# Kernel tuning notes

Hardware: AMD Instinct MI355X
Metric: run time of the kernel (lower is better)

Reference implementation:

```python
import jax, jax.numpy as jnp
import numpy as np

B, S, N = 8, 512, 2048   # batch, seq_len (=input_dim=output_dim), num_features (graph nodes)
HID = 512
K = 8                    # k_neighbors


def _construct_adj(x, k):
    """Faithful port of construct_graph: note the original normalizes the
    (1, N) mean-feature vector along dim=1 (whole-vector L2 norm), so the
    'similarity matrix' is actually the outer product v v^T / ||v||^2."""
    Bn, Sn, Nn = x.shape
    fv = x.mean(axis=1)                                  # (B, N)
    nf = fv / jnp.linalg.norm(fv, axis=1, keepdims=True)  # whole-row L2 normalize
    sim = nf[:, :, None] * nf[:, None, :]                # (B, N, N) outer product
    kk = min(k, Nn - 1)
    _, idx = jax.lax.top_k(sim, kk + 1)                  # (B, N, kk+1)
    idx = idx[..., 1:]                                   # drop the single largest (B, N, kk)
    b_ix = jnp.arange(Bn)[:, None, None]
    r_ix = jnp.arange(Nn)[None, :, None]
    adj = jnp.zeros((Bn, Nn, Nn), x.dtype).at[b_ix, r_ix, idx].set(1.0)
    adj = jnp.maximum(adj, jnp.swapaxes(adj, 1, 2))      # symmetrize (adj[idx, i] = 1)
    d = jnp.arange(Nn)
    adj = adj.at[:, d, d].set(1.0)                       # fill_diagonal_(1)
    return adj


def _gc(x, adj, W, b):
    """GraphConvLayer: degree-normalized adjacency bmm after linear."""
    deg = adj.sum(axis=2, keepdims=True)                 # (B, N, 1)
    deg = jnp.where(deg == 0, jnp.ones_like(deg), deg)
    h = x @ W.T + b                                      # (B, N, out)
    return jnp.einsum('bij,bjh->bih', adj / deg, h)


def setup_inputs() -> dict:
    key = jax.random.key(0)
    k0, k1, k2 = jax.random.split(key, 3)
    x = jax.random.normal(k0, (B, S, N), jnp.float32)
    W1 = jax.random.normal(k1, (HID, S), jnp.float32) * 0.02
    b1 = jnp.zeros((HID,), jnp.float32)
    W2 = jax.random.normal(k2, (S, HID), jnp.float32) * 0.02
    b2 = jnp.zeros((S,), jnp.float32)
    return {"x": x, "W1": W1, "b1": b1, "W2": W2, "b2": b2}


def reference(x, W1, b1, W2, b2):
    adj = _construct_adj(x, K)                           # (B, N, N)
    xr = jnp.swapaxes(x, 1, 2)                           # (B, N, S)
    h = jax.nn.relu(_gc(xr, adj, W1, b1))                # (B, N, HID); dropout is eval no-op
    h = _gc(h, adj, W2, b2)                              # (B, N, S)
    return jnp.swapaxes(h, 1, 2)                         # (B, S, N)
```

## Files before the change

kernel.cpp:

```cpp
#include <hip/hip_runtime.h>
#include <hip/hip_bf16.h>
#include <cstdint>

typedef unsigned short u16;
typedef __bf16 bf16x8 __attribute__((ext_vector_type(8)));
typedef float f32x4 __attribute__((ext_vector_type(4)));
typedef float f32x8 __attribute__((ext_vector_type(8)));
typedef unsigned short u16x4 __attribute__((ext_vector_type(4)));
typedef unsigned short u16x8 __attribute__((ext_vector_type(8)));

#define BB 8
#define SS 512
#define NN 2048
#define HH 512
#define MM (BB*NN)

__device__ inline u16 f2b(float f) {
  __hip_bfloat16 h = __float2bfloat16(f);
  return *reinterpret_cast<u16*>(&h);
}
__device__ inline float b2f(u16 u) {
  unsigned x = ((unsigned)u) << 16;
  return __uint_as_float(x);
}
__device__ inline f32x8 b2f8(u16x8 v) {
  f32x8 r;
  #pragma unroll
  for (int k = 0; k < 8; ++k) r[k] = b2f(v[k]);
  return r;
}

#define GLOAD16(g, l) __builtin_amdgcn_global_load_lds( \
    (const __attribute__((address_space(1))) void*)(g), \
    (__attribute__((address_space(3))) void*)(l), 16, 0, 0)

__device__ inline void remap_mn(int bid, int& m0, int& n0) {
  const int xcd = bid & 7, k = bid >> 3;
  m0 = (xcd * 16 + (k >> 2)) * 128;
  n0 = (k & 3) * 128;
}

__global__ __launch_bounds__(256) void k_prep(const float* __restrict__ x, u16* __restrict__ xr,
                       float* __restrict__ fvp,
                       const float* __restrict__ W1, const float* __restrict__ W2,
                       u16* __restrict__ w1b, u16* __restrict__ w2b,
                       float* __restrict__ xs ) {
  const int u = blockIdx.x;
  const int tid = threadIdx.x;
  if (u < 4096) {
    __shared__ float t[64][33];
    __shared__ float ps[8][32];
    const int tx = tid & 31, ty = tid >> 5;
    const int n0 = (u & 63) * 32, st = (u >> 6) & 7, b = u >> 9;
    const int s0 = st * 64;
    float acc = 0.f;
    #pragma unroll
    for (int i = ty; i < 64; i += 8) {
      float w = x[(size_t)b*SS*NN + (size_t)(s0+i)*NN + n0 + tx];
      t[i][tx] = w; acc += w;
    }
    ps[ty][tx] = acc;
    __syncthreads();
    if (ty == 0) {
      float s = 0.f;
      #pragma unroll
      for (int j = 0; j < 8; ++j) s += ps[j][tx];
      fvp[((size_t)(b*8 + st))*NN + n0 + tx] = s;
    }
    const int wtx = tid & 15, wty = tid >> 4;
    #pragma unroll
    for (int j = wty; j < 32; j += 16) {
      ushort4 o;
      o.x = f2b(t[wtx*4+0][j]); o.y = f2b(t[wtx*4+1][j]);
      o.z = f2b(t[wtx*4+2][j]); o.w = f2b(t[wtx*4+3][j]);
      *(ushort4*)(xr + ((size_t)b*NN + n0 + j)*SS + s0 + wtx*4) = o;
    }
    if (u < 96) {
      ((float4*)xs)[u*256 + tid] = make_float4(0.f, 0.f, 0.f, 0.f);
    }
  } else {
    const int b2v = u - 4096;
    const float* Wsrc = (b2v >= 256) ? W2 : W1;
    u16* wb = (b2v >= 256) ? w2b : w1b;
    const int off = (b2v & 255) * 1024;
    float4 v = ((const float4*)(Wsrc + off))[tid];
    ushort4 o; o.x = f2b(v.x); o.y = f2b(v.y); o.z = f2b(v.z); o.w = f2b(v.w);
    *(ushort4*)(wb + off + tid*4) = o;
  }
}

__global__ __launch_bounds__(256) void k_tops(const float* __restrict__ fvp, const u16* __restrict__ xr,
                       int* __restrict__ meta, int* __restrict__ rowfl, float* __restrict__ xs) {
  const int tid = threadIdx.x;
  if (blockIdx.x < BB) {
    const int b = blockIdx.x;
    __shared__ float v[NN];
    __shared__ unsigned long long wk[8];
    __shared__ unsigned long long winner[2];
    __shared__ int sel[18];
    __shared__ int scnt[12];
    __shared__ int ccnt[12];
    const int wv = tid >> 6, ln = tid & 63;

    float lv[8];
    {
      f32x4 a0 = {0,0,0,0}, a1 = {0,0,0,0};
      for (int sb_ = 0; sb_ < 8; ++sb_) {
        const f32x4* p = (const f32x4*)(fvp + ((size_t)(b*8 + sb_))*NN + tid*8);
        a0 += p[0]; a1 += p[1];
      }
      lv[0]=a0[0]; lv[1]=a0[1]; lv[2]=a0[2]; lv[3]=a0[3];
      lv[4]=a1[0]; lv[5]=a1[1]; lv[6]=a1[2]; lv[7]=a1[3];
    }
    #pragma unroll
    for (int j = 0; j < 8; ++j) v[tid*8+j] = lv[j];

    unsigned long long kD[8], kA[8];
    #pragma unroll
    for (int j = 0; j < 8; ++j) {
      unsigned u = __float_as_uint(lv[j]);
      u = (u & 0x80000000u) ? ~u : (u | 0x80000000u);
      unsigned idx = (unsigned)(tid*8 + j);
      kD[j] = ((unsigned long long)u << 32) | (0xFFFFFFFFu - idx);
      kA[j] = ((unsigned long long)(~u) << 32) | (0xFFFFFFFFu - idx);
    }
    unsigned mskD = 0, mskA = 0;
    for (int r = 0; r < 9; ++r) {
      unsigned long long bD = 0ull, bA = 0ull;
      #pragma unroll
      for (int j = 0; j < 8; ++j) {
        if (!((mskD >> j) & 1) && kD[j] > bD) bD = kD[j];
        if (!((mskA >> j) & 1) && kA[j] > bA) bA = kA[j];
      }
      #pragma unroll
      for (int o = 32; o > 0; o >>= 1) {
        unsigned long long oD = __shfl_xor(bD, o, 64);
        unsigned long long oA = __shfl_xor(bA, o, 64);
        if (oD > bD) bD = oD;
        if (oA > bA) bA = oA;
      }
      if (ln == 0) { wk[wv] = bD; wk[4+wv] = bA; }
      __syncthreads();
      if (tid == 0) {
        unsigned long long mD = wk[0], mA = wk[4];
        #pragma unroll
        for (int q = 1; q < 4; ++q) {
          if (wk[q] > mD) mD = wk[q];
          if (wk[4+q] > mA) mA = wk[4+q];
        }
        winner[0] = mD; winner[1] = mA;
        sel[r]   = (int)(0xFFFFFFFFu - (unsigned)mD);
        sel[9+r] = (int)(0xFFFFFFFFu - (unsigned)mA);
      }
      __syncthreads();
      unsigned iD = 0xFFFFFFFFu - (unsigned)winner[0];
      unsigned iA = 0xFFFFFFFFu - (unsigned)winner[1];
      if ((int)(iD >> 3) == tid) mskD |= 1u << (iD & 7);
      if ((int)(iA >> 3) == tid) mskA |= 1u << (iA & 7);
    }

    int cp = 0, cn = 0, cz = 0;
    #pragma unroll
    for (int j = 0; j < 8; ++j) { cp += (lv[j] > 0.f); cn += (lv[j] < 0.f); cz += (lv[j] == 0.f); }
    #pragma unroll
    for (int o = 32; o > 0; o >>= 1) { cp += __shfl_xor(cp, o, 64); cn += __shfl_xor(cn, o, 64); cz += __shfl_xor(cz, o, 64); }
    if (ln == 0) { ccnt[wv] = cp; ccnt[4+wv] = cn; ccnt[8+wv] = cz; }
    __syncthreads();
    if (tid == 0) {
      int CP = 0, CN = 0, CZ = 0;
      #pragma unroll
      for (int q = 0; q < 4; ++q) { CP += ccnt[q]; CN += ccnt[4+q]; CZ += ccnt[8+q]; }
      scnt[0] = CP; scnt[1] = CN; scnt[2] = CZ;
      for (int t2 = 3; t2 < 12; ++t2) scnt[t2] = 0;
      for (int r = 1; r < 9; ++r) {
        float wD = v[sel[r]];   scnt[3] += (wD > 0.f); scnt[4] += (wD < 0.f); scnt[5] += (wD == 0.f);
        float wA = v[sel[9+r]]; scnt[6] += (wA > 0.f); scnt[7] += (wA < 0.f); scnt[8] += (wA == 0.f);
        float wZ = v[r];        scnt[9] += (wZ > 0.f); scnt[10] += (wZ < 0.f); scnt[11] += (wZ == 0.f);
      }
    }
    __syncthreads();
    #pragma unroll
    for (int j = 0; j < 8; ++j) {
      const int i = tid*8 + j;
      float w = lv[j];
      int cls = (w > 0.f) ? 0 : ((w < 0.f) ? 1 : 2);
      int mD = 0, mA = 0;
      #pragma unroll
      for (int r = 1; r < 9; ++r) { mD |= (sel[r] == i); mA |= (sel[9+r] == i); }
      int mZ8 = (i >= 1 && i <= 8);
      rowfl[b*NN + i] = cls | (mD << 2) | (mA << 3) | (mZ8 << 4);
    }
    if (tid < 18) meta[b*32 + tid] = sel[tid];
    if (tid >= 18 && tid < 30) meta[b*32 + tid] = scnt[tid - 18];
    __syncthreads();
    #pragma unroll
    for (int half = 0; half < 2; ++half) {
      const int d = tid + half*256;
      float a[9];
      #pragma unroll
      for (int q = 0; q < 9; ++q) a[q] = 0.f;
      for (int r = 1; r < 9; ++r) {
        int iD = sel[r];   float wD = v[iD]; int cD = (wD>0.f)?0:((wD<0.f)?1:2);
        float vD = b2f(xr[((size_t)b*NN + iD)*512 + d]);
        int iA = sel[9+r]; float wA = v[iA]; int cA = (wA>0.f)?0:((wA<0.f)?1:2);
        float vA = b2f(xr[((size_t)b*NN + iA)*512 + d]);
        float wZ = v[r];   int cZ = (wZ>0.f)?0:((wZ<0.f)?1:2);
        float vZ = b2f(xr[((size_t)b*NN + r)*512 + d]);
        #pragma unroll
        for (int q = 0; q < 3; ++q) {
          a[q]   += (cD == q) ? vD : 0.f;
          a[3+q] += (cA == q) ? vA : 0.f;
          a[6+q] += (cZ == q) ? vZ : 0.f;
        }
      }
      #pragma unroll
      for (int q = 0; q < 9; ++q) xs[((size_t)b*12 + 3 + q)*512 + d] = a[q];
    }
  } else {
    const int u = blockIdx.x - 8, b = u >> 5, c = u & 31, n0 = c*64;
    __shared__ f32x8 red[12][64];
    __shared__ int scls[64];
    if (tid < 64) {
      float s = 0.f;
      for (int sb_ = 0; sb_ < 8; ++sb_) s += fvp[((size_t)(b*8 + sb_))*NN + n0 + tid];
      scls[tid] = (s > 0.f) ? 0 : ((s < 0.f) ? 1 : 2);
    }
    __syncthreads();
    const int fc = tid & 63, rg = tid >> 6;
    f32x8 sp = {0,0,0,0,0,0,0,0}, sn = sp, sz = sp;
    for (int it = 0; it < 16; ++it) {
      const int nr = rg + it*4;
      const int cls = scls[nr];
      f32x8 hf = b2f8(*(const u16x8*)(xr + ((size_t)b*NN + n0 + nr)*512 + fc*8));
      if (cls == 0) sp += hf; else if (cls == 1) sn += hf; else sz += hf;
    }
    red[0*4+rg][fc] = sp; red[1*4+rg][fc] = sn; red[2*4+rg][fc] = sz;
    __syncthreads();
    if (rg == 0) {
      sp = red[0][fc] + red[1][fc] + red[2][fc] + red[3][fc];
      sn = red[4][fc] + red[5][fc] + red[6][fc] + red[7][fc];
      sz = red[8][fc] + red[9][fc] + red[10][fc] + red[11][fc];
      #pragma unroll
      for (int j = 0; j < 8; ++j) {
        atomicAdd(&xs[((size_t)b*12 + 0)*512 + fc*8 + j], sp[j]);
        atomicAdd(&xs[((size_t)b*12 + 1)*512 + fc*8 + j], sn[j]);
        atomicAdd(&xs[((size_t)b*12 + 2)*512 + fc*8 + j], sz[j]);
      }
    }
  }
}

__global__ __launch_bounds__(256) void k_sums(const u16* __restrict__ g1, const int* __restrict__ meta,
                      const int* __restrict__ rowfl, float* __restrict__ g1s) {
  const int tid = threadIdx.x;
  if (blockIdx.x < BB) {
    const int b = blockIdx.x;
    const int* mb = meta + b*32;
    #pragma unroll
    for (int half = 0; half < 2; ++half) {
      const int d = tid + half*256;
      float a[9];
      #pragma unroll
      for (int q = 0; q < 9; ++q) a[q] = 0.f;
      for (int r = 1; r < 9; ++r) {
        int iD = mb[r];   int cD = rowfl[b*NN + iD] & 3;
        float vD = b2f(g1[((size_t)b*NN + iD)*512 + d]);
        int iA = mb[9+r]; int cA = rowfl[b*NN + iA] & 3;
        float vA = b2f(g1[((size_t)b*NN + iA)*512 + d]);
        int cZ = rowfl[b*NN + r] & 3;
        float vZ = b2f(g1[((size_t)b*NN + r)*512 + d]);
        #pragma unroll
        for (int q = 0; q < 3; ++q) {
          a[q]   += (cD == q) ? vD : 0.f;
          a[3+q] += (cA == q) ? vA : 0.f;
          a[6+q] += (cZ == q) ? vZ : 0.f;
        }
      }
      #pragma unroll
      for (int q = 0; q < 9; ++q) g1s[((size_t)b*12 + 3 + q)*512 + d] = a[q];
    }
  } else {
    const int u = blockIdx.x - 8, b = u >> 5, c = u & 31, n0 = c*64;
    __shared__ f32x8 red[12][64];
    __shared__ int scls[64];
    if (tid < 64) scls[tid] = rowfl[b*NN + n0 + tid] & 3;
    __syncthreads();
    const int fc = tid & 63, rg = tid >> 6;
    f32x8 sp = {0,0,0,0,0,0,0,0}, sn = sp, sz = sp;
    for (int it = 0; it < 16; ++it) {
      const int nr = rg + it*4;
      const int cls = scls[nr];
      f32x8 hf = b2f8(*(const u16x8*)(g1 + ((size_t)b*NN + n0 + nr)*512 + fc*8));
      if (cls == 0) sp += hf; else if (cls == 1) sn += hf; else sz += hf;
    }
    red[0*4+rg][fc] = sp; red[1*4+rg][fc] = sn; red[2*4+rg][fc] = sz;
    __syncthreads();
    if (rg == 0) {
      sp = red[0][fc] + red[1][fc] + red[2][fc] + red[3][fc];
      sn = red[4][fc] + red[5][fc] + red[6][fc] + red[7][fc];
      sz = red[8][fc] + red[9][fc] + red[10][fc] + red[11][fc];
      #pragma unroll
      for (int j = 0; j < 8; ++j) {
        atomicAdd(&g1s[((size_t)b*12 + 0)*512 + fc*8 + j], sp[j]);
        atomicAdd(&g1s[((size_t)b*12 + 1)*512 + fc*8 + j], sn[j]);
        atomicAdd(&g1s[((size_t)b*12 + 2)*512 + fc*8 + j], sz[j]);
      }
    }
  }
}

template<int MODE>
__global__ __launch_bounds__(256, 2) void k_gemmf(const u16* __restrict__ A, const u16* __restrict__ Bw,
                       const float* __restrict__ bias, const float* __restrict__ sums,
                       const int* __restrict__ meta, const int* __restrict__ rowfl,
                       void* __restrict__ outp) {
  __shared__ __align__(16) char SM[33152];
  u16* As  = (u16*)SM;
  u16* Bs  = (u16*)(SM + 8192);
  u16* xsb = (u16*)(SM + 16384);
  int* cnt = (int*)(SM + 33088);
  const int tid = threadIdx.x;
  const int w = tid >> 6, l = tid & 63;
  const int wm = w >> 1, wn = w & 1;
  int m0, n0; remap_mn(blockIdx.x, m0, n0);
  const int b = m0 >> 11;

  for (int i = tid; i < 12*512; i += 256) {
    const int s = i >> 9, k = i & 511;
    xsb[s*520 + k] = f2b(sums[(size_t)b*12*512 + i]);
  }
  for (int i = tid; i < 4*520; i += 256) xsb[12*520 + i] = 0;
  if (tid < 12) cnt[tid] = meta[b*32 + 18 + tid];

  f32x4 acc[4][4]; f32x4 accV[4];
  #pragma unroll
  for (int i = 0; i < 4; ++i) {
    accV[i] = (f32x4){0.f, 0.f, 0.f, 0.f};
    #pragma unroll
    for (int j = 0; j < 4; ++j) acc[i][j] = (f32x4){0.f, 0.f, 0.f, 0.f};
  }
  const int srow = l >> 2;
  const int sslot = (l & 3) ^ ((l >> 3) & 3);
  const int skk = sslot * 8;
  const int lr = l & 15;
  const int g = l >> 4;
  const int lkA = ((g ^ ((lr >> 1) & 3)) * 8);
  const int lk = g * 8;
  for (int kt = 0; kt < 512; kt += 32) {
    #pragma unroll
    for (int p = 0; p < 2; ++p) {
      const int q = w*2 + p;
      GLOAD16(A  + (size_t)(m0 + q*16 + srow)*512 + kt + skk, As + q*512);
      GLOAD16(Bw + (size_t)(n0 + q*16 + srow)*512 + kt + skk, Bs + q*512);
    }
    __syncthreads();
    bf16x8 af[4], bfr[4];
    #pragma unroll
    for (int i = 0; i < 4; ++i) af[i] = *(const bf16x8*)(As + (wm*64 + i*16 + lr)*32 + lkA);
    #pragma unroll
    for (int j = 0; j < 4; ++j) bfr[j] = *(const bf16x8*)(Bs + (wn*64 + j*16 + lr)*32 + lkA);
    #pragma unroll
    for (int i = 0; i < 4; ++i)
      #pragma unroll
      for (int j = 0; j < 4; ++j)
        acc[i][j] = __builtin_amdgcn_mfma_f32_16x16x32_bf16(bfr[j], af[i], acc[i][j], 0, 0, 0);
    if (wm == 0) {
      bf16x8 afx = *(const bf16x8*)(xsb + lr*520 + kt + lk);
      #pragma unroll
      for (int j = 0; j < 4; ++j)
        accV[j] = __builtin_amdgcn_mfma_f32_16x16x32_bf16(afx, bfr[j], accV[j], 0, 0, 0);
    }
    __syncthreads();
  }

  float* Vl = (float*)SM;
  if (wm == 0) {
    #pragma unroll
    for (int j = 0; j < 4; ++j) {
      const int c = wn*64 + j*16 + lr;
      const float bv = bias[n0 + c];
      #pragma unroll
      for (int r = 0; r < 4; ++r) {
        const int s = (l >> 4)*4 + r;
        if (s < 12) Vl[s*128 + c] = accV[j][r] + (float)cnt[s] * bv;
      }
    }
  }
  __syncthreads();

  int fl[4]; float rdg[4]; bool cs[4];
  const float* Vb[4];
  #pragma unroll
  for (int i = 0; i < 4; ++i) {
    const int m = m0 + wm*64 + i*16 + lr;
    const int f = rowfl[m];
    fl[i] = f;
    const int cls = f & 3;
    const int bD = (f >> 2) & 1, bA = (f >> 3) & 1, bZ = (f >> 4) & 1;
    const int rb = 3 + cls*3;
    const int c3c = bD*cnt[0] + bA*cnt[1] + bZ*cnt[2];
    const int c2c = cnt[rb] + cnt[rb+1] + cnt[rb+2] - bD*cnt[rb] - bA*cnt[rb+1] - bZ*cnt[rb+2];
    cs[i] = (cls == 0 && bD) || (cls == 1 && bA) || (cls == 2 && bZ);
    float deg = (float)(c3c + c2c) + (cs[i] ? 0.f : 1.f);
    if (deg < 1.f) deg = 1.f;
    rdg[i] = 1.f / deg;
    Vb[i] = Vl + rb*128;
  }

  if (MODE == 0) {
    u16* G = (u16*)outp;
    #pragma unroll
    for (int j = 0; j < 4; ++j) {
      const int dgb = n0 + wn*64 + j*16 + (l >> 4)*4;
      u16x4 o[4];
      #pragma unroll
      for (int r = 0; r < 4; ++r) {
        const int c = wn*64 + j*16 + (l >> 4)*4 + r;
        const float bv = bias[dgb + r];
        const float v0 = Vl[c], v1 = Vl[128 + c], v2 = Vl[256 + c];
        #pragma unroll
        for (int i = 0; i < 4; ++i) {
          const int f = fl[i];
          const float t0 = Vb[i][c], t1 = Vb[i][128 + c], t2 = Vb[i][256 + c];
          float c3 = ((f&4)?v0:0.f) + ((f&8)?v1:0.f) + ((f&16)?v2:0.f);
          float c2 = t0 + t1 + t2
                   - ((f&4)?t0:0.f) - ((f&8)?t1:0.f) - ((f&16)?t2:0.f);
          float val = (c3 + c2) * rdg[i];
          if (!cs[i]) val += (acc[i][j][r] + bv) * rdg[i];
          o[i][r] = f2b(fmaxf(val, 0.f));
        }
      }
      #pragma unroll
      for (int i = 0; i < 4; ++i)
        *(u16x4*)(G + (size_t)(m0 + wm*64 + i*16 + lr)*512 + dgb) = o[i];
    }
  } else {
    float* out = (float*)outp;
    float (*ep)[130] = (float(*)[130])(SM + 8192);
    const int nloc = m0 & 2047;
    for (int j = 0; j < 4; ++j) {
      #pragma unroll
      for (int r = 0; r < 4; ++r) {
        const int c = wn*64 + j*16 + (l >> 4)*4 + r;
        const float bv = bias[n0 + c];
        const float v0 = Vl[c], v1 = Vl[128 + c], v2 = Vl[256 + c];
        #pragma unroll
        for (int i = 0; i < 4; ++i) {
          const int f = fl[i];
          const float t0 = Vb[i][c], t1 = Vb[i][128 + c], t2 = Vb[i][256 + c];
          float c3 = ((f&4)?v0:0.f) + ((f&8)?v1:0.f) + ((f&16)?v2:0.f);
          float c2 = t0 + t1 + t2
                   - ((f&4)?t0:0.f) - ((f&8)?t1:0.f) - ((f&16)?t2:0.f);
          float val = (c3 + c2) * rdg[i];
          if (!cs[i]) val += (acc[i][j][r] + bv) * rdg[i];
          ep[wn*16 + (l >> 4)*4 + r][wm*64 + i*16 + lr] = val;
        }
      }
      __syncthreads();
      #pragma unroll
      for (int rr = 0; rr < 8; ++rr) {
        const int q = w*8 + rr;
        const int s = n0 + (q >> 4)*64 + j*16 + (q & 15);
        float2 v2 = *(const float2*)&ep[q][2*l];
        *(float2*)(out + ((size_t)b*SS + s)*NN + nloc + 2*l) = v2;
      }
      __syncthreads();
    }
  }
}

extern "C" void kernel_launch(void* const* d_in, const int* in_sizes, int n_in,
                              void* d_out, int out_size, void* d_ws, size_t ws_size,
                              hipStream_t stream) {
  const float* x  = (const float*)d_in[0];
  const float* W1 = (const float*)d_in[1];
  const float* b1 = (const float*)d_in[2];
  const float* W2 = (const float*)d_in[3];
  const float* b2 = (const float*)d_in[4];
  float* out = (float*)d_out;
  char* ws = (char*)d_ws;

  float* fvp   = (float*)(ws + 0);
  int*   meta  = (int*)  (ws + 1048576);
  int*   rowfl = (int*)  (ws + 1049600);
  float* xs    = (float*)(ws + 1115136);
  float* g1s   = (float*)(ws + 1311744);
  u16*   w1b   = (u16*)  (ws + 1508352);
  u16*   w2b   = (u16*)  (ws + 2032640);
  u16*   g1    = (u16*)  (ws + 2556928);
  u16*   xr    = (u16*)  (ws + 19334144);

  k_prep<<<4608, 256, 0, stream>>>(x, xr, fvp, W1, W2, w1b, w2b, xs);
  k_tops<<<264, 256, 0, stream>>>(fvp, xr, meta, rowfl, xs);
  k_gemmf<0><<<512, 256, 0, stream>>>(xr, w1b, b1, xs, meta, rowfl, (void*)g1);
  k_sums<<<264, 256, 0, stream>>>(g1, meta, rowfl, g1s);
  k_gemmf<1><<<512, 256, 0, stream>>>(g1, w2b, b2, g1s, meta, rowfl, (void*)out);
}
```

Measured before the change: 112.9 us.

## Fuse class-sum reduction of first graph-conv output into GEMM epilogue

Removes the separate k_sums kernel, which re-read the whole bf16 hidden activation g1 to build per-class and per-neighbor column sums. The first GEMM's epilogue now builds these sums from the post-ReLU values it already holds in registers. It uses wave shuffles, a shared-memory stage and global atomicAdds into g1s. This saves a kernel launch and a full pass over g1, at the cost of extra atomics and epilogue work. It also depends on g1s rows 3-11 being zeroed beforehand, since they are now accumulated rather than overwritten.

Measured after the change: 97.56 us. 13.6% less time.

```diff
diff --git a/kernel.cpp b/kernel.cpp
--- a/kernel.cpp
+++ b/kernel.cpp
@@ -250,70 +250,11 @@
   }
 }
 
-__global__ __launch_bounds__(256) void k_sums(const u16* __restrict__ g1, const int* __restrict__ meta,
-                      const int* __restrict__ rowfl, float* __restrict__ g1s) {
-  const int tid = threadIdx.x;
-  if (blockIdx.x < BB) {
-    const int b = blockIdx.x;
-    const int* mb = meta + b*32;
-    #pragma unroll
-    for (int half = 0; half < 2; ++half) {
-      const int d = tid + half*256;
-      float a[9];
-      #pragma unroll
-      for (int q = 0; q < 9; ++q) a[q] = 0.f;
-      for (int r = 1; r < 9; ++r) {
-        int iD = mb[r];   int cD = rowfl[b*NN + iD] & 3;
-        float vD = b2f(g1[((size_t)b*NN + iD)*512 + d]);
-        int iA = mb[9+r]; int cA = rowfl[b*NN + iA] & 3;
-        float vA = b2f(g1[((size_t)b*NN + iA)*512 + d]);
-        int cZ = rowfl[b*NN + r] & 3;
-        float vZ = b2f(g1[((size_t)b*NN + r)*512 + d]);
-        #pragma unroll
-        for (int q = 0; q < 3; ++q) {
-          a[q]   += (cD == q) ? vD : 0.f;
-          a[3+q] += (cA == q) ? vA : 0.f;
-          a[6+q] += (cZ == q) ? vZ : 0.f;
-        }
-      }
-      #pragma unroll
-      for (int q = 0; q < 9; ++q) g1s[((size_t)b*12 + 3 + q)*512 + d] = a[q];
-    }
-  } else {
-    const int u = blockIdx.x - 8, b = u >> 5, c = u & 31, n0 = c*64;
-    __shared__ f32x8 red[12][64];
-    __shared__ int scls[64];
-    if (tid < 64) scls[tid] = rowfl[b*NN + n0 + tid] & 3;
-    __syncthreads();
-    const int fc = tid & 63, rg = tid >> 6;
-    f32x8 sp = {0,0,0,0,0,0,0,0}, sn = sp, sz = sp;
-    for (int it = 0; it < 16; ++it) {
-      const int nr = rg + it*4;
-      const int cls = scls[nr];
-      f32x8 hf = b2f8(*(const u16x8*)(g1 + ((size_t)b*NN + n0 + nr)*512 + fc*8));
-      if (cls == 0) sp += hf; else if (cls == 1) sn += hf; else sz += hf;
-    }
-    red[0*4+rg][fc] = sp; red[1*4+rg][fc] = sn; red[2*4+rg][fc] = sz;
-    __syncthreads();
-    if (rg == 0) {
-      sp = red[0][fc] + red[1][fc] + red[2][fc] + red[3][fc];
-      sn = red[4][fc] + red[5][fc] + red[6][fc] + red[7][fc];
-      sz = red[8][fc] + red[9][fc] + red[10][fc] + red[11][fc];
-      #pragma unroll
-      for (int j = 0; j < 8; ++j) {
-        atomicAdd(&g1s[((size_t)b*12 + 0)*512 + fc*8 + j], sp[j]);
-        atomicAdd(&g1s[((size_t)b*12 + 1)*512 + fc*8 + j], sn[j]);
-        atomicAdd(&g1s[((size_t)b*12 + 2)*512 + fc*8 + j], sz[j]);
-      }
-    }
-  }
-}
-
 template<int MODE>
 __global__ __launch_bounds__(256, 2) void k_gemmf(const u16* __restrict__ A, const u16* __restrict__ Bw,
                        const float* __restrict__ bias, const float* __restrict__ sums,
                        const int* __restrict__ meta, const int* __restrict__ rowfl,
-                       void* __restrict__ outp) {
+                       void* __restrict__ outp, float* __restrict__ osum) {
   __shared__ __align__(16) char SM[33152];
   u16* As  = (u16*)SM;
   u16* Bs  = (u16*)(SM + 8192);
@@ -409,15 +350,17 @@
 
   if (MODE == 0) {
     u16* G = (u16*)outp;
+    float* cbin = (float*)(SM + 8192);
     #pragma unroll
     for (int j = 0; j < 4; ++j) {
-      const int dgb = n0 + wn*64 + j*16 + (l >> 4)*4;
+      const int dgb = n0 + wn*64 + j*16 + g*4;
       u16x4 o[4];
       #pragma unroll
       for (int r = 0; r < 4; ++r) {
-        const int c = wn*64 + j*16 + (l >> 4)*4 + r;
+        const int c = wn*64 + j*16 + g*4 + r;
         const float bv = bias[dgb + r];
         const float v0 = Vl[c], v1 = Vl[128 + c], v2 = Vl[256 + c];
+        float s0 = 0.f, s1 = 0.f, s2 = 0.f;
         #pragma unroll
         for (int i = 0; i < 4; ++i) {
           const int f = fl[i];
@@ -427,12 +370,43 @@
                    - ((f&4)?t0:0.f) - ((f&8)?t1:0.f) - ((f&16)?t2:0.f);
           float val = (c3 + c2) * rdg[i];
           if (!cs[i]) val += (acc[i][j][r] + bv) * rdg[i];
-          o[i][r] = f2b(fmaxf(val, 0.f));
+          val = fmaxf(val, 0.f);
+          o[i][r] = f2b(val);
+          const int cls = f & 3;
+          s0 += (cls == 0) ? val : 0.f;
+          s1 += (cls == 1) ? val : 0.f;
+          s2 += (cls == 2) ? val : 0.f;
+          if (f & 0x1C) {
+            if (f & 4)  atomicAdd(&osum[(size_t)(b*12 + 3 + cls)*512 + dgb + r], val);
+            if (f & 8)  atomicAdd(&osum[(size_t)(b*12 + 6 + cls)*512 + dgb + r], val);
+            if (f & 16) atomicAdd(&osum[(size_t)(b*12 + 9 + cls)*512 + dgb + r], val);
+          }
+        }
+        #pragma unroll
+        for (int o2 = 1; o2 < 16; o2 <<= 1) {
+          s0 += __shfl_xor(s0, o2, 64);
+          s1 += __shfl_xor(s1, o2, 64);
+          s2 += __shfl_xor(s2, o2, 64);
+        }
+        if (lr == 0) {
+          float* cb = cbin + (((wm*2 + wn)*4 + g)*16 + (j*4 + r))*3;
+          cb[0] = s0; cb[1] = s1; cb[2] = s2;
         }
       }
       #pragma unroll
       for (int i = 0; i < 4; ++i)
         *(u16x4*)(G + (size_t)(m0 + wm*64 + i*16 + lr)*512 + dgb) = o[i];
+    }
+    __syncthreads();
+    for (int item = tid; item < 384; item += 256) {
+      const int wg = item / 48;
+      const int rem = item % 48;
+      const int jr = rem / 3, cls = rem % 3;
+      const int wnn = wg >> 2, gg = wg & 3;
+      const int c = wnn*64 + (jr >> 2)*16 + gg*4 + (jr & 3);
+      const float vsum = cbin[(((0*2 + wnn)*4 + gg)*16 + jr)*3 + cls]
+                       + cbin[(((1*2 + wnn)*4 + gg)*16 + jr)*3 + cls];
+      atomicAdd(&osum[(size_t)(b*12 + cls)*512 + n0 + c], vsum);
     }
   } else {
     float* out = (float*)outp;
@@ -441,7 +415,7 @@
     for (int j = 0; j < 4; ++j) {
       #pragma unroll
       for (int r = 0; r < 4; ++r) {
-        const int c = wn*64 + j*16 + (l >> 4)*4 + r;
+        const int c = wn*64 + j*16 + g*4 + r;
         const float bv = bias[n0 + c];
         const float v0 = Vl[c], v1 = Vl[128 + c], v2 = Vl[256 + c];
         #pragma unroll
@@ -453,7 +427,7 @@
                    - ((f&4)?t0:0.f) - ((f&8)?t1:0.f) - ((f&16)?t2:0.f);
           float val = (c3 + c2) * rdg[i];
           if (!cs[i]) val += (acc[i][j][r] + bv) * rdg[i];
-          ep[wn*16 + (l >> 4)*4 + r][wm*64 + i*16 + lr] = val;
+          ep[wn*16 + g*4 + r][wm*64 + i*16 + lr] = val;
         }
       }
       __syncthreads();
@@ -492,7 +466,6 @@
 
   k_prep<<<4608, 256, 0, stream>>>(x, xr, fvp, W1, W2, w1b, w2b, xs);
   k_tops<<<264, 256, 0, stream>>>(fvp, xr, meta, rowfl, xs);
-  k_gemmf<0><<<512, 256, 0, stream>>>(xr, w1b, b1, xs, meta, rowfl, (void*)g1);
-  k_sums<<<264, 256, 0, stream>>>(g1, meta, rowfl, g1s);
-  k_gemmf<1><<<512, 256, 0, stream>>>(g1, w2b, b2, g1s, meta, rowfl, (void*)out);
-}
+  k_gemmf<0><<<512, 256, 0, stream>>>(xr, w1b, b1, xs, meta, rowfl, (void*)g1, g1s);
+  k_gemmf<1><<<512, 256, 0, stream>>>(g1, w2b, b2, g1s, meta, rowfl, (void*)out, nullptr);
+}
```
